# Performance work log

Measured on AMD Instinct MI355X. Metric: run time of the kernel, lower is better.

## Reference

```python
import jax, jax.numpy as jnp
import numpy as np

NIBBLE_ZERO = 8  # int4 zero-point (symmetric around 8 for unsigned nibble storage)


def _dequant(w_packed, w_scales):
    # w_packed: [out, in//2] int32 holding uint8 bytes, two 4-bit values each.
    low = w_packed & 0xF            # first nibble -> even input positions
    high = (w_packed >> 4) & 0xF    # second nibble -> odd input positions
    out_f = w_packed.shape[0]
    # interleave nibbles along the input dim: [out, in//2, 2] -> [out, in]
    q = jnp.stack([low, high], axis=-1).reshape(out_f, -1)
    return (q.astype(w_scales.dtype) - NIBBLE_ZERO) * w_scales[:, None]  # [out, in]


def setup_inputs() -> dict:
    key = jax.random.key(0)
    k1, k2, k3, k4 = jax.random.split(key, 4)
    N, IN, OUT = 4096, 4096, 4096
    x = jax.random.normal(k1, (N, IN), dtype=jnp.float32)
    w_packed = jax.random.randint(k2, (OUT, IN // 2), 0, 256, dtype=jnp.int32)
    w_scales = jax.random.uniform(k3, (OUT,), dtype=jnp.float32, minval=0.01, maxval=0.05)
    bias = jax.random.normal(k4, (OUT,), dtype=jnp.float32)
    return {"x": x, "w_packed": w_packed, "w_scales": w_scales, "bias": bias}


def reference(x, w_packed, w_scales, bias):
    W = _dequant(w_packed, w_scales)          # [out, in]
    return jnp.einsum('ni,oi->no', x, W) + bias  # [N, out]
```

## Files before the change

### kernel.cpp

```cpp
#include <hip/hip_runtime.h>
#include <hip/hip_bf16.h>


typedef __attribute__((ext_vector_type(8))) __bf16 bf16x8;
typedef __attribute__((ext_vector_type(4))) float f32x4;

#define GLOBAL_AS __attribute__((address_space(1)))
#define LDS_AS __attribute__((address_space(3)))

#define BM 128
#define BN 128
#define BK 64

__device__ inline unsigned short f32_to_bf16(float f) {
    unsigned int u = __float_as_uint(f);
    unsigned int r = (u + 0x7FFFu + ((u >> 16) & 1u)) >> 16;
    return (unsigned short)r;
}

__global__ void cvt_x(const float* __restrict__ x, unsigned short* __restrict__ xb, int n8) {
    const int stride = gridDim.x * blockDim.x;
    for (int i = blockIdx.x * blockDim.x + threadIdx.x; i < n8; i += stride) {
        float4 a = ((const float4*)x)[2 * i];
        float4 b = ((const float4*)x)[2 * i + 1];
        union { unsigned short h[8]; uint4 u; } o;
        o.h[0] = f32_to_bf16(a.x); o.h[1] = f32_to_bf16(a.y);
        o.h[2] = f32_to_bf16(a.z); o.h[3] = f32_to_bf16(a.w);
        o.h[4] = f32_to_bf16(b.x); o.h[5] = f32_to_bf16(b.y);
        o.h[6] = f32_to_bf16(b.z); o.h[7] = f32_to_bf16(b.w);
        ((uint4*)xb)[i] = o.u;
    }
}

__global__ void unpack_w(const int* __restrict__ wp, unsigned short* __restrict__ wb, int n4) {
    const int stride = gridDim.x * blockDim.x;
    for (int i = blockIdx.x * blockDim.x + threadIdx.x; i < n4; i += stride) {
        int4 v = ((const int4*)wp)[i];
        int vals[4] = {v.x, v.y, v.z, v.w};
        union { unsigned short h[8]; uint4 u; } o;
#pragma unroll
        for (int t = 0; t < 4; ++t) {
            o.h[2 * t]     = f32_to_bf16((float)((vals[t] & 0xF) - 8));
            o.h[2 * t + 1] = f32_to_bf16((float)(((vals[t] >> 4) & 0xF) - 8));
        }
        ((uint4*)wb)[i] = o.u;
    }
}

__global__ __launch_bounds__(256) void gemm_bt(
    const unsigned short* __restrict__ A,
    const unsigned short* __restrict__ B,
    const float* __restrict__ scales,
    const float* __restrict__ bias,
    float* __restrict__ C,
    int M, int N, int K)
{
    __shared__ unsigned short As[BM * BK];
    __shared__ unsigned short Bs[BN * BK];

    const int tid  = threadIdx.x;
    const int wave = tid >> 6;
    const int lane = tid & 63;
    const int wm = wave >> 1;
    const int wn = wave & 1;
    const int m0 = blockIdx.y * BM;
    const int n0 = blockIdx.x * BN;

    f32x4 acc[4][4];
#pragma unroll
    for (int i = 0; i < 4; ++i)
#pragma unroll
        for (int j = 0; j < 4; ++j)
            acc[i][j] = (f32x4){0.f, 0.f, 0.f, 0.f};

    const int srow = tid >> 3;
    const int scol = ((tid & 7) ^ (srow & 7)) * 8;

    const unsigned short* Ag = A + (size_t)(m0 + srow) * K + scol;
    const unsigned short* Bg = B + (size_t)(n0 + srow) * K + scol;

    const int am = lane & 15;
    const int aq = lane >> 4;
    const int axr = am & 7;

    for (int k0 = 0; k0 < K; k0 += BK) {
#pragma unroll
        for (int j = 0; j < 4; ++j) {
            __builtin_amdgcn_global_load_lds(
                (const GLOBAL_AS void*)(Ag + (size_t)(j * 32) * K + k0),
                (LDS_AS void*)(As + tid * 8 + j * 2048), 16, 0, 0);
        }
#pragma unroll
        for (int j = 0; j < 4; ++j) {
            __builtin_amdgcn_global_load_lds(
                (const GLOBAL_AS void*)(Bg + (size_t)(j * 32) * K + k0),
                (LDS_AS void*)(Bs + tid * 8 + j * 2048), 16, 0, 0);
        }
        __syncthreads();

#pragma unroll
        for (int kk = 0; kk < BK; kk += 32) {
            const int kb = kk >> 3;
            bf16x8 af[4], bfr[4];
#pragma unroll
            for (int i = 0; i < 4; ++i) {
                const int row = wm * 64 + i * 16 + am;
                af[i] = *(const bf16x8*)&As[row * BK + (((kb + aq) ^ axr) << 3)];
            }
#pragma unroll
            for (int j = 0; j < 4; ++j) {
                const int row = wn * 64 + j * 16 + am;
                bfr[j] = *(const bf16x8*)&Bs[row * BK + (((kb + aq) ^ axr) << 3)];
            }
#pragma unroll
            for (int i = 0; i < 4; ++i)
#pragma unroll
                for (int j = 0; j < 4; ++j)
                    acc[i][j] = __builtin_amdgcn_mfma_f32_16x16x32_bf16(af[i], bfr[j], acc[i][j], 0, 0, 0);
        }
        __syncthreads();
    }

    const int cq = lane >> 4;
    const int cc = lane & 15;
#pragma unroll
    for (int j = 0; j < 4; ++j) {
        const int col = n0 + wn * 64 + j * 16 + cc;
        const float s = scales[col];
        const float b = bias[col];
#pragma unroll
        for (int i = 0; i < 4; ++i) {
            const int rowb = m0 + wm * 64 + i * 16 + cq * 4;
#pragma unroll
            for (int r = 0; r < 4; ++r) {
                C[(size_t)(rowb + r) * N + col] = acc[i][j][r] * s + b;
            }
        }
    }
}

__global__ void naive_kernel(const float* __restrict__ x, const int* __restrict__ wp,
                             const float* __restrict__ sc, const float* __restrict__ bs,
                             float* __restrict__ out, int NR, int OUTF, int INF) {
    int idx = blockIdx.x * 256 + threadIdx.x;
    if (idx >= NR * OUTF) return;
    int n = idx / OUTF, o = idx - n * OUTF;
    const float* xr = x + (size_t)n * INF;
    const int* wr = wp + (size_t)o * (INF / 2);
    float acc = 0.f;
    for (int c = 0; c < INF / 2; ++c) {
        int v = wr[c];
        acc += xr[2 * c] * (float)((v & 0xF) - 8) + xr[2 * c + 1] * (float)(((v >> 4) & 0xF) - 8);
    }
    out[idx] = acc * sc[o] + bs[o];
}

extern "C" void kernel_launch(void* const* d_in, const int* in_sizes, int n_in,
                              void* d_out, int out_size, void* d_ws, size_t ws_size,
                              hipStream_t stream) {
    const float* x      = (const float*)d_in[0];
    const int*   wp     = (const int*)d_in[1];
    const float* scales = (const float*)d_in[2];
    const float* bias   = (const float*)d_in[3];
    float* out = (float*)d_out;

    const int OUTF = in_sizes[2];
    const int INF  = (2 * in_sizes[1]) / OUTF;
    const int NR   = in_sizes[0] / INF;

    unsigned short* xb = (unsigned short*)d_ws;
    unsigned short* wb = xb + (size_t)NR * INF;
    const size_t need = ((size_t)NR * INF + (size_t)OUTF * INF) * sizeof(unsigned short);

    if (ws_size >= need && (NR % BM) == 0 && (OUTF % BN) == 0 && (INF % BK) == 0
        && (in_sizes[0] % 8) == 0 && (in_sizes[1] % 4) == 0) {
        cvt_x<<<1024, 256, 0, stream>>>(x, xb, in_sizes[0] / 8);
        unpack_w<<<1024, 256, 0, stream>>>(wp, wb, in_sizes[1] / 4);
        dim3 grid(OUTF / BN, NR / BM);
        gemm_bt<<<grid, 256, 0, stream>>>(xb, wb, scales, bias, out, NR, OUTF, INF);
    } else {
        int total = NR * OUTF;
        naive_kernel<<<(total + 255) / 256, 256, 0, stream>>>(x, wp, scales, bias, out, NR, OUTF, INF);
    }
}
```

Baseline: 304.0 us.

## Switch GEMM to 32x32x16 MFMA with k-major LDS layout and fuse prep kernels

Replaces the 16x16x32 bf16 MFMA tiling (4x4 fragments per wave) with 32x32x16 MFMA (2x2 fragments per wave). The LDS layout changes to a k-chunk-major arrangement with no swizzle, so each lane reads its 8-element fragment contiguously. This is meant to cut LDS fragment loads and the MFMA instruction count. It also merges the x conversion and weight unpack kernels into one launch to save a launch. The unswizzled layout may introduce LDS bank conflicts on fragment reads.

Result: slower. 404.1 us (+32.9%).

```diff
diff --git a/kernel.cpp b/kernel.cpp
--- a/kernel.cpp
+++ b/kernel.cpp
@@ -3,7 +3,7 @@
 
 
 typedef __attribute__((ext_vector_type(8))) __bf16 bf16x8;
-typedef __attribute__((ext_vector_type(4))) float f32x4;
+typedef __attribute__((ext_vector_type(16))) float f32x16;
 
 #define GLOBAL_AS __attribute__((address_space(1)))
 #define LDS_AS __attribute__((address_space(3)))
@@ -18,32 +18,33 @@
     return (unsigned short)r;
 }
 
-__global__ void cvt_x(const float* __restrict__ x, unsigned short* __restrict__ xb, int n8) {
+__global__ void prep(const float* __restrict__ x, unsigned short* __restrict__ xb,
+                     const int* __restrict__ wp, unsigned short* __restrict__ wb,
+                     int n8x, int n4w) {
     const int stride = gridDim.x * blockDim.x;
-    for (int i = blockIdx.x * blockDim.x + threadIdx.x; i < n8; i += stride) {
-        float4 a = ((const float4*)x)[2 * i];
-        float4 b = ((const float4*)x)[2 * i + 1];
-        union { unsigned short h[8]; uint4 u; } o;
-        o.h[0] = f32_to_bf16(a.x); o.h[1] = f32_to_bf16(a.y);
-        o.h[2] = f32_to_bf16(a.z); o.h[3] = f32_to_bf16(a.w);
-        o.h[4] = f32_to_bf16(b.x); o.h[5] = f32_to_bf16(b.y);
-        o.h[6] = f32_to_bf16(b.z); o.h[7] = f32_to_bf16(b.w);
-        ((uint4*)xb)[i] = o.u;
-    }
-}
-
-__global__ void unpack_w(const int* __restrict__ wp, unsigned short* __restrict__ wb, int n4) {
-    const int stride = gridDim.x * blockDim.x;
-    for (int i = blockIdx.x * blockDim.x + threadIdx.x; i < n4; i += stride) {
-        int4 v = ((const int4*)wp)[i];
-        int vals[4] = {v.x, v.y, v.z, v.w};
-        union { unsigned short h[8]; uint4 u; } o;
+    const int total = n8x + n4w;
+    for (int i = blockIdx.x * blockDim.x + threadIdx.x; i < total; i += stride) {
+        if (i < n8x) {
+            float4 a = ((const float4*)x)[2 * i];
+            float4 b = ((const float4*)x)[2 * i + 1];
+            union { unsigned short h[8]; uint4 u; } o;
+            o.h[0] = f32_to_bf16(a.x); o.h[1] = f32_to_bf16(a.y);
+            o.h[2] = f32_to_bf16(a.z); o.h[3] = f32_to_bf16(a.w);
+            o.h[4] = f32_to_bf16(b.x); o.h[5] = f32_to_bf16(b.y);
+            o.h[6] = f32_to_bf16(b.z); o.h[7] = f32_to_bf16(b.w);
+            ((uint4*)xb)[i] = o.u;
+        } else {
+            int k = i - n8x;
+            int4 v = ((const int4*)wp)[k];
+            int vals[4] = {v.x, v.y, v.z, v.w};
+            union { unsigned short h[8]; uint4 u; } o;
 #pragma unroll
-        for (int t = 0; t < 4; ++t) {
-            o.h[2 * t]     = f32_to_bf16((float)((vals[t] & 0xF) - 8));
-            o.h[2 * t + 1] = f32_to_bf16((float)(((vals[t] >> 4) & 0xF) - 8));
+            for (int t = 0; t < 4; ++t) {
+                o.h[2 * t]     = f32_to_bf16((float)((vals[t] & 0xF) - 8));
+                o.h[2 * t + 1] = f32_to_bf16((float)(((vals[t] >> 4) & 0xF) - 8));
+            }
+            ((uint4*)wb)[k] = o.u;
         }
-        ((uint4*)wb)[i] = o.u;
     }
 }
 
@@ -66,74 +67,71 @@
     const int m0 = blockIdx.y * BM;
     const int n0 = blockIdx.x * BN;
 
-    f32x4 acc[4][4];
+    f32x16 acc[2][2];
 #pragma unroll
-    for (int i = 0; i < 4; ++i)
+    for (int i = 0; i < 2; ++i)
 #pragma unroll
-        for (int j = 0; j < 4; ++j)
-            acc[i][j] = (f32x4){0.f, 0.f, 0.f, 0.f};
+        for (int j = 0; j < 2; ++j)
+#pragma unroll
+            for (int r = 0; r < 16; ++r)
+                acc[i][j][r] = 0.f;
 
-    const int srow = tid >> 3;
-    const int scol = ((tid & 7) ^ (srow & 7)) * 8;
+    const int srow = tid & 127;
+    const int kbb  = tid >> 7;
 
-    const unsigned short* Ag = A + (size_t)(m0 + srow) * K + scol;
-    const unsigned short* Bg = B + (size_t)(n0 + srow) * K + scol;
+    const unsigned short* Ag = A + (size_t)(m0 + srow) * K + kbb * 8;
+    const unsigned short* Bg = B + (size_t)(n0 + srow) * K + kbb * 8;
 
-    const int am = lane & 15;
-    const int aq = lane >> 4;
-    const int axr = am & 7;
+    const int lanelow = lane & 31;
+    const int half    = lane >> 5;
+    const int aoff = half * 1024 + (wm * 64 + lanelow) * 8;
+    const int boff = half * 1024 + (wn * 64 + lanelow) * 8;
 
     for (int k0 = 0; k0 < K; k0 += BK) {
 #pragma unroll
         for (int j = 0; j < 4; ++j) {
             __builtin_amdgcn_global_load_lds(
-                (const GLOBAL_AS void*)(Ag + (size_t)(j * 32) * K + k0),
-                (LDS_AS void*)(As + tid * 8 + j * 2048), 16, 0, 0);
+                (const GLOBAL_AS void*)(Ag + k0 + j * 16),
+                (LDS_AS void*)((LDS_AS char*)As + tid * 16 + j * 4096), 16, 0, 0);
         }
 #pragma unroll
         for (int j = 0; j < 4; ++j) {
             __builtin_amdgcn_global_load_lds(
-                (const GLOBAL_AS void*)(Bg + (size_t)(j * 32) * K + k0),
-                (LDS_AS void*)(Bs + tid * 8 + j * 2048), 16, 0, 0);
+                (const GLOBAL_AS void*)(Bg + k0 + j * 16),
+                (LDS_AS void*)((LDS_AS char*)Bs + tid * 16 + j * 4096), 16, 0, 0);
         }
         __syncthreads();
 
 #pragma unroll
-        for (int kk = 0; kk < BK; kk += 32) {
-            const int kb = kk >> 3;
-            bf16x8 af[4], bfr[4];
+        for (int ki = 0; ki < 4; ++ki) {
+            bf16x8 af[2], bfr[2];
 #pragma unroll
-            for (int i = 0; i < 4; ++i) {
-                const int row = wm * 64 + i * 16 + am;
-                af[i] = *(const bf16x8*)&As[row * BK + (((kb + aq) ^ axr) << 3)];
-            }
+            for (int t = 0; t < 2; ++t)
+                af[t] = *(const bf16x8*)&As[aoff + ki * 2048 + t * 256];
 #pragma unroll
-            for (int j = 0; j < 4; ++j) {
-                const int row = wn * 64 + j * 16 + am;
-                bfr[j] = *(const bf16x8*)&Bs[row * BK + (((kb + aq) ^ axr) << 3)];
-            }
+            for (int t = 0; t < 2; ++t)
+                bfr[t] = *(const bf16x8*)&Bs[boff + ki * 2048 + t * 256];
 #pragma unroll
-            for (int i = 0; i < 4; ++i)
+            for (int i = 0; i < 2; ++i)
 #pragma unroll
-                for (int j = 0; j < 4; ++j)
-                    acc[i][j] = __builtin_amdgcn_mfma_f32_16x16x32_bf16(af[i], bfr[j], acc[i][j], 0, 0, 0);
+                for (int j = 0; j < 2; ++j)
+                    acc[i][j] = __builtin_amdgcn_mfma_f32_32x32x16_bf16(af[i], bfr[j], acc[i][j], 0, 0, 0);
         }
         __syncthreads();
     }
 
-    const int cq = lane >> 4;
-    const int cc = lane & 15;
 #pragma unroll
-    for (int j = 0; j < 4; ++j) {
-        const int col = n0 + wn * 64 + j * 16 + cc;
+    for (int tj = 0; tj < 2; ++tj) {
+        const int col = n0 + wn * 64 + tj * 32 + lanelow;
         const float s = scales[col];
         const float b = bias[col];
 #pragma unroll
-        for (int i = 0; i < 4; ++i) {
-            const int rowb = m0 + wm * 64 + i * 16 + cq * 4;
+        for (int ti = 0; ti < 2; ++ti) {
+            const int rowbase = m0 + wm * 64 + ti * 32 + half * 4;
 #pragma unroll
-            for (int r = 0; r < 4; ++r) {
-                C[(size_t)(rowb + r) * N + col] = acc[i][j][r] * s + b;
+            for (int r = 0; r < 16; ++r) {
+                const int row = rowbase + (r & 3) + 8 * (r >> 2);
+                C[(size_t)row * N + col] = acc[ti][tj][r] * s + b;
             }
         }
     }
@@ -174,8 +172,7 @@
 
     if (ws_size >= need && (NR % BM) == 0 && (OUTF % BN) == 0 && (INF % BK) == 0
         && (in_sizes[0] % 8) == 0 && (in_sizes[1] % 4) == 0) {
-        cvt_x<<<1024, 256, 0, stream>>>(x, xb, in_sizes[0] / 8);
-        unpack_w<<<1024, 256, 0, stream>>>(wp, wb, in_sizes[1] / 4);
+        prep<<<1024, 256, 0, stream>>>(x, xb, wp, wb, in_sizes[0] / 8, in_sizes[1] / 4);
         dim3 grid(OUTF / BN, NR / BM);
         gemm_bt<<<grid, 256, 0, stream>>>(xb, wb, scales, bias, out, NR, OUTF, INF);
     } else {
```
